# Kernel tuning notes

Hardware: AMD Instinct MI355X
Metric: run time of the kernel (lower is better)

The kernel has to match this reference:

```python
import jax, jax.numpy as jnp
import numpy as np

NUM_PM = 254
NUM_VM = 768
SEQ = NUM_PM + NUM_VM + 2  # 1024
H = 8
D = 256
DH = D // H
FF = 1024
L = 3
B = 8
PM_COV = 16
VM_COV = 16


def _ln(x, g, b, eps=1e-5):
    m = jnp.mean(x, axis=-1, keepdims=True)
    v = jnp.mean((x - m) ** 2, axis=-1, keepdims=True)
    return (x - m) * jax.lax.rsqrt(v + eps) * g + b


def setup_inputs() -> dict:
    key = jax.random.key(0)
    ks = jax.random.split(key, 32)
    n = lambda k, s: (jax.random.normal(k, s, dtype=jnp.float32) * 0.02)
    return {
        "vm_states": jax.random.normal(ks[0], (B, NUM_VM, VM_COV), dtype=jnp.float32),
        "num_step_states": jax.random.uniform(ks[1], (B, 1, 1), dtype=jnp.float32),
        "pm_states": jax.random.normal(ks[2], (B, NUM_PM, PM_COV), dtype=jnp.float32),
        "vm_pm_relation": jax.random.randint(ks[3], (B, SEQ - 2, 1), 0, NUM_PM),
        "num_vms_mask": jnp.zeros((B, NUM_VM), dtype=bool),
        "pm_W": n(ks[4], (PM_COV, D)), "pm_b": jnp.zeros((D,), jnp.float32),
        "vm_W": n(ks[5], (VM_COV, D)), "vm_b": jnp.zeros((D,), jnp.float32),
        "Wqkv": n(ks[6], (L, D, 3 * D)), "bqkv": jnp.zeros((L, 3 * D), jnp.float32),
        "Wo": n(ks[7], (L, D, D)), "bo": jnp.zeros((L, D), jnp.float32),
        "ln1_g": jnp.ones((L, D), jnp.float32), "ln1_b": jnp.zeros((L, D), jnp.float32),
        "ln2_g": jnp.ones((L, D), jnp.float32), "ln2_b": jnp.zeros((L, D), jnp.float32),
        "W1": n(ks[8], (L, D, FF)), "b1": jnp.zeros((L, FF), jnp.float32),
        "W2": n(ks[9], (L, FF, D)), "b2": jnp.zeros((L, D), jnp.float32),
        "out_W": n(ks[10], (D, 1)), "out_b": jnp.zeros((1,), jnp.float32),
        "crit_W": n(ks[11], (D, 1)), "crit_b": jnp.zeros((1,), jnp.float32),
    }


def reference(vm_states, num_step_states, pm_states, vm_pm_relation, num_vms_mask,
              pm_W, pm_b, vm_W, vm_b, Wqkv, bqkv, Wo, bo,
              ln1_g, ln1_b, ln2_g, ln2_b, W1, b1, W2, b2,
              out_W, out_b, crit_W, crit_b):
    b = vm_states.shape[0]
    # --- relation-based sparse mask: True = blocked ---
    r = vm_pm_relation[:, :, 0]                              # [b, SEQ-2]
    inner = r[:, :, None] != r[:, None, :]                   # [b, SEQ-2, SEQ-2]
    local = jnp.ones((b, SEQ, SEQ), dtype=bool)
    local = local.at[:, 0, 0].set(False)
    local = local.at[:, -1, -1].set(False)
    local = local.at[:, 1:-1, 1:-1].set(inner)
    pad = jnp.zeros((b, SEQ), dtype=bool).at[:, 1 + NUM_PM:-1].set(num_vms_mask)
    bias = jnp.where(local | pad[:, None, :], -1e9, 0.0)[:, None]  # [b,1,SEQ,SEQ]
    # --- encode ---
    src = jnp.concatenate([jnp.tile(num_step_states, (1, 1, D)),
                           pm_states @ pm_W + pm_b], axis=1)       # [b, NUM_PM+1, D]
    critic_tok = -jnp.ones((b, 1, D), dtype=vm_states.dtype)
    tgt = jnp.concatenate([vm_states @ vm_W + vm_b, critic_tok], axis=1)  # [b, NUM_VM+1, D]
    x = jnp.concatenate([src, tgt], axis=1)                   # [b, SEQ, D]
    scale = 1.0 / np.sqrt(DH)
    for i in range(L):
        # pre-norm masked self-attention
        h = _ln(x, ln1_g[i], ln1_b[i])
        qkv = h @ Wqkv[i] + bqkv[i]
        q, k, v = [t.reshape(b, SEQ, H, DH) for t in jnp.split(qkv, 3, axis=-1)]
        scores = jnp.einsum('bqhd,bkhd->bhqk', q, k) * scale + bias
        attn = jax.nn.softmax(scores, axis=-1)
        o = jnp.einsum('bhqk,bkhd->bqhd', attn, v).reshape(b, SEQ, D)
        x = x + o @ Wo[i] + bo[i]
        # pre-norm gelu FFN
        h2 = _ln(x, ln2_g[i], ln2_b[i])
        x = x + jax.nn.gelu(h2 @ W1[i] + b1[i]) @ W2[i] + b2[i]
    tgt_out = x[:, NUM_PM + 1:]                               # [b, NUM_VM+1, D]
    score = (tgt_out[:, :-1] @ out_W + out_b)[..., 0]         # [b, NUM_VM]
    critic_score = tgt_out[:, -1] @ crit_W + crit_b           # [b, 1]
    return jnp.concatenate([score, critic_score], axis=1)     # [b, NUM_VM+1]
```

## Files before the change

### kernel.cpp

```cpp
#include <hip/hip_runtime.h>
#include <hip/hip_bf16.h>
#include <math.h>

#define NUM_PM 254
#define NUM_VM 768
#define SEQQ   1024
#define NH     8
#define DD     256
#define DH     32
#define FF     1024
#define NB     8
#define MROWS  (NB*SEQQ)

typedef unsigned short u16;
typedef __attribute__((ext_vector_type(8))) short bf16x8;
typedef __attribute__((ext_vector_type(4))) float f32x4;

__device__ __forceinline__ float bf2f(u16 u){
    union { float f; unsigned int i; } c; c.i = ((unsigned int)u) << 16; return c.f;
}
__device__ __forceinline__ u16 f2bf(float f){
    union { float f; unsigned int u; } c; c.f = f;
    unsigned int r = c.u + 0x7FFFu + ((c.u >> 16) & 1u);
    return (u16)(r >> 16);
}
__device__ __forceinline__ float gelu_tanh(float x){
    float x3 = x*x*x;
    float t = tanhf(0.7978845608028654f*(x + 0.044715f*x3));
    return 0.5f*x*(1.0f+t);
}

#define GLOAD16(gp, lp) __builtin_amdgcn_global_load_lds( \
    (const __attribute__((address_space(1))) void*)(gp), \
    (__attribute__((address_space(3))) void*)(lp), 16, 0, 0)

__global__ void prologue_kernel(const float* __restrict__ Wqkv, const float* __restrict__ Wo,
                                const float* __restrict__ W1,   const float* __restrict__ W2,
                                u16* __restrict__ wq, u16* __restrict__ wo,
                                u16* __restrict__ w1, u16* __restrict__ w2,
                                const int* __restrict__ rel, const unsigned char* __restrict__ mask,
                                int* __restrict__ kcnt, int* __restrict__ koff, int* __restrict__ kmem,
                                int* __restrict__ pcnt, int* __restrict__ poff, int* __restrict__ pmem,
                                const float* __restrict__ vm_states,
                                const float* __restrict__ num_step,
                                const float* __restrict__ pm_states,
                                const float* __restrict__ pm_W, const float* __restrict__ pm_b,
                                const float* __restrict__ vm_W, const float* __restrict__ vm_b,
                                const float* __restrict__ g, const float* __restrict__ beta,
                                float* __restrict__ x, u16* __restrict__ h,
                                float* __restrict__ outz)
{
    __shared__ float t[32][33];
    __shared__ int cntS[256], offS[256], wsum4[4];
    __shared__ int memS[1040];
    int bid = blockIdx.x;
    int tid = threadIdx.x;
    if (bid < 2304){
        int id = bid;
        const float* in; u16* out; int K, N, layer, tile;
        if (id < 576)       { in=Wqkv; out=wq; K=256;  N=768;  layer=id/192; tile=id%192; }
        else if (id < 768)  { id-=576;  in=Wo; out=wo; K=256;  N=256;  layer=id/64;  tile=id%64;  }
        else if (id < 1536) { id-=768;  in=W1; out=w1; K=256;  N=1024; layer=id/256; tile=id%256; }
        else                { id-=1536; in=W2; out=w2; K=1024; N=256;  layer=id/256; tile=id%256; }
        int ntx = N/32;
        int n0 = (tile % ntx)*32, k0 = (tile / ntx)*32;
        size_t lofs = (size_t)layer * K * N;
        int tx = tid & 31, ty = tid >> 5;
        #pragma unroll
        for (int i=0;i<4;i++)
            t[ty + i*8][tx] = in[lofs + (size_t)(k0 + ty + i*8)*N + n0 + tx];
        __syncthreads();
        #pragma unroll
        for (int i=0;i<4;i++)
            out[lofs + (size_t)(n0 + ty + i*8)*K + k0 + tx] = f2bf(t[tx][ty + i*8]);
    } else if (bid < 2312){
        int b = bid - 2304;
        cntS[tid] = 0;
        __syncthreads();
        int myc[4], myp[4];
        bool mykey[4];
        #pragma unroll
        for (int si=0; si<4; si++){
            int s = si*256 + tid;
            bool mid = (s != 0) && (s != SEQQ-1);
            myc[si] = -1; mykey[si] = false;
            if (mid){
                int cc = rel[b*(SEQQ-2) + s-1];
                myc[si] = cc;
                bool masked = (s >= 1+NUM_PM) && mask[b*NUM_VM + (s-1-NUM_PM)];
                if (!masked){ mykey[si] = true; myp[si] = atomicAdd(&cntS[cc], 1); }
            }
        }
        __syncthreads();
        {
            int v = cntS[tid];
            int incl = v;
            #pragma unroll
            for (int d=1; d<64; d<<=1){
                int n = __shfl_up(incl, d);
                if ((tid & 63) >= d) incl += n;
            }
            offS[tid] = incl - v;
            if ((tid & 63) == 63) wsum4[tid>>6] = incl;
        }
        __syncthreads();
        {
            int w = tid >> 6, base = 0;
            #pragma unroll
            for (int i=0;i<4;i++) if (i < w) base += wsum4[i];
            offS[tid] += base;
        }
        __syncthreads();
        #pragma unroll
        for (int si=0; si<4; si++){
            if (mykey[si]){
                int s = si*256 + tid;
                int pos = offS[myc[si]] + myp[si];
                memS[pos] = s;
                kmem[b*SEQQ + pos] = s;
            }
        }
        kcnt[b*256 + tid] = cntS[tid];
        koff[b*256 + tid] = offS[tid];
        __syncthreads();
        #pragma unroll
        for (int si=0; si<4; si++){
            int s = si*256 + tid;
            if (myc[si] >= 0){
                int c = myc[si];
                int cnt = cntS[c], off = offS[c];
                pcnt[b*SEQQ + s] = cnt;
                poff[b*SEQQ + s] = b*SEQQ + off;
                int mrow[16];
                #pragma unroll
                for (int j=0;j<16;j++)
                    mrow[j] = (j < cnt) ? memS[off + j] : s;
                int4* prow = (int4*)&pmem[(size_t)(b*SEQQ + s)*16];
                prow[0] = (int4){mrow[0], mrow[1], mrow[2], mrow[3]};
                prow[1] = (int4){mrow[4], mrow[5], mrow[6], mrow[7]};
                prow[2] = (int4){mrow[8], mrow[9], mrow[10],mrow[11]};
                prow[3] = (int4){mrow[12],mrow[13],mrow[14],mrow[15]};
            }
        }
        #pragma unroll
        for (int si=0; si<4; si++){
            int idx = si*256 + tid;
            if (idx < 769) outz[b*769 + idx] = 0.f;
        }
    } else {
        int row = (bid - 2312)*4 + (tid>>6);
        int lane = tid & 63;
        int b = row >> 10, s = row & 1023;
        int col = lane*4;
        float4 out;
        if (s == 0){
            float v = num_step[b]; out = (float4){v,v,v,v};
        } else if (s == SEQQ-1){
            out = (float4){-1.f,-1.f,-1.f,-1.f};
        } else {
            const float* in; const float* W; const float* bias;
            if (s <= NUM_PM){ in = pm_states + (size_t)(b*NUM_PM + s-1)*16; W = pm_W; bias = pm_b; }
            else            { in = vm_states + (size_t)(b*NUM_VM + (s-1-NUM_PM))*16; W = vm_W; bias = vm_b; }
            float4 i0 = *(const float4*)in,      i1 = *(const float4*)(in+4);
            float4 i2 = *(const float4*)(in+8),  i3 = *(const float4*)(in+12);
            float in16[16] = {i0.x,i0.y,i0.z,i0.w, i1.x,i1.y,i1.z,i1.w,
                              i2.x,i2.y,i2.z,i2.w, i3.x,i3.y,i3.z,i3.w};
            out = *(const float4*)&bias[col];
            #pragma unroll
            for (int k=0;k<16;k++){
                float4 w4 = *(const float4*)&W[k*DD + col];
                out.x = fmaf(in16[k], w4.x, out.x);
                out.y = fmaf(in16[k], w4.y, out.y);
                out.z = fmaf(in16[k], w4.z, out.z);
                out.w = fmaf(in16[k], w4.w, out.w);
            }
        }
        *(float4*)&x[(size_t)row*DD + col] = out;
        float s1 = out.x+out.y+out.z+out.w;
        float s2 = fmaf(out.x,out.x, fmaf(out.y,out.y, fmaf(out.z,out.z, out.w*out.w)));
        #pragma unroll
        for (int off=1; off<64; off<<=1){ s1 += __shfl_xor(s1,off); s2 += __shfl_xor(s2,off); }
        float m    = s1*(1.0f/DD);
        float var  = s2*(1.0f/DD) - m*m;
        float rstd = rsqrtf(var + 1e-5f);
        float4 g4 = *(const float4*)&g[col];
        float4 b4 = *(const float4*)&beta[col];
        short4 o;
        o.x = (short)f2bf((out.x-m)*rstd*g4.x + b4.x);
        o.y = (short)f2bf((out.y-m)*rstd*g4.y + b4.y);
        o.z = (short)f2bf((out.z-m)*rstd*g4.z + b4.z);
        o.w = (short)f2bf((out.w-m)*rstd*g4.w + b4.w);
        *(short4*)&h[(size_t)row*DD + col] = o;
    }
}

__global__ void ln_kernel(const float* __restrict__ x, const float* __restrict__ g,
                          const float* __restrict__ bta, u16* __restrict__ out)
{
    int row = blockIdx.x*4 + (threadIdx.x>>6);
    int lane = threadIdx.x & 63;
    const float4 v = *(const float4*)&x[(size_t)row*DD + lane*4];
    float s1 = v.x+v.y+v.z+v.w;
    float s2 = fmaf(v.x,v.x, fmaf(v.y,v.y, fmaf(v.z,v.z, v.w*v.w)));
    #pragma unroll
    for (int off=1; off<64; off<<=1){ s1 += __shfl_xor(s1,off); s2 += __shfl_xor(s2,off); }
    float m    = s1*(1.0f/DD);
    float var  = s2*(1.0f/DD) - m*m;
    float rstd = rsqrtf(var + 1e-5f);
    float4 g4 = *(const float4*)&g[lane*4];
    float4 b4 = *(const float4*)&bta[lane*4];
    short4 o;
    o.x = (short)f2bf((v.x-m)*rstd*g4.x + b4.x);
    o.y = (short)f2bf((v.y-m)*rstd*g4.y + b4.y);
    o.z = (short)f2bf((v.z-m)*rstd*g4.z + b4.z);
    o.w = (short)f2bf((v.w-m)*rstd*g4.w + b4.w);
    *(short4*)&out[(size_t)row*DD + lane*4] = o;
}

__launch_bounds__(256)
__global__ void qgemm_kernel(const u16* __restrict__ A, const u16* __restrict__ Bt,
                             const float* __restrict__ bias, u16* __restrict__ C,
                             int N, int K)
{
    __shared__ u16 As[2][64][32];
    __shared__ u16 Bs[2][128][32];
    int tid = threadIdx.x;
    int wid = tid >> 6, lane = tid & 63;
    int wr = wid >> 1, wc = wid & 1;
    int row0 = blockIdx.y*64, col0 = blockIdx.x*128;
    int l15 = lane & 15, lh = lane >> 4;

    const u16* Ag = A  + (size_t)(row0 + wid*16 + (lane>>2))*K + (lane&3)*8;
    const u16* Bg = Bt + (size_t)(col0 + wid*32 + (lane>>2))*K + (lane&3)*8;

#define STAGE_Q(buf, k0) do{ \
    GLOAD16(Ag + (k0),          &As[buf][wid*16][0]);    \
    GLOAD16(Bg + (k0),          &Bs[buf][wid*32][0]);    \
    GLOAD16(Bg + (k0) + 16*K,   &Bs[buf][wid*32+16][0]); }while(0)

    f32x4 acc[2][4] = {};
    int nk = K >> 5;
    STAGE_Q(0, 0);
    __syncthreads();
    for (int kt = 0; kt < nk; kt++){
        int cur = kt & 1;
        if (kt+1 < nk) STAGE_Q(cur^1, (kt+1)*32);
        bf16x8 af[2], bfv[4];
        #pragma unroll
        for (int i=0;i<2;i++)
            af[i] = *(const bf16x8*)&As[cur][wr*32 + i*16 + l15][lh*8];
        #pragma unroll
        for (int j=0;j<4;j++)
            bfv[j] = *(const bf16x8*)&Bs[cur][wc*64 + j*16 + l15][lh*8];
        #pragma unroll
        for (int i=0;i<2;i++)
            #pragma unroll
            for (int j=0;j<4;j++)
                acc[i][j] = __builtin_amdgcn_mfma_f32_16x16x32_bf16(af[i], bfv[j], acc[i][j], 0,0,0);
        __syncthreads();
    }
#undef STAGE_Q

    #pragma unroll
    for (int i=0;i<2;i++){
        #pragma unroll
        for (int j=0;j<4;j++){
            int col = col0 + wc*64 + j*16 + l15;
            float bb = bias[col];
            #pragma unroll
            for (int r=0;r<4;r++){
                int row = row0 + wr*32 + i*16 + lh*4 + r;
                C[(size_t)row*N + col] = f2bf(acc[i][j][r] + bb);
            }
        }
    }
}

__launch_bounds__(256)
__global__ void mgemm_kernel(const u16* __restrict__ A, const u16* __restrict__ Bt,
                             const float* __restrict__ bias, u16* __restrict__ C,
                             int N, int K)
{
    __shared__ u16 As[2][128][32];
    __shared__ u16 Bs[2][128][32];
    int tid = threadIdx.x;
    int wid = tid >> 6, lane = tid & 63;
    int wr = wid >> 1, wc = wid & 1;
    int row0 = blockIdx.y*128, col0 = blockIdx.x*128;
    int l15 = lane & 15, lh = lane >> 4;

    const u16* Ag = A  + (size_t)(row0 + wid*32 + (lane>>2))*K + (lane&3)*8;
    const u16* Bg = Bt + (size_t)(col0 + wid*32 + (lane>>2))*K + (lane&3)*8;

#define STAGE_M(buf, k0) do{ \
    GLOAD16(Ag + (k0),          &As[buf][wid*32][0]);    \
    GLOAD16(Ag + (k0) + 16*K,   &As[buf][wid*32+16][0]); \
    GLOAD16(Bg + (k0),          &Bs[buf][wid*32][0]);    \
    GLOAD16(Bg + (k0) + 16*K,   &Bs[buf][wid*32+16][0]); }while(0)

    f32x4 acc[4][4] = {};
    int nk = K >> 5;
    STAGE_M(0, 0);
    __syncthreads();
    for (int kt = 0; kt < nk; kt++){
        int cur = kt & 1;
        if (kt+1 < nk) STAGE_M(cur^1, (kt+1)*32);
        bf16x8 af[4], bfv[4];
        #pragma unroll
        for (int f=0; f<4; f++){
            af[f]  = *(const bf16x8*)&As[cur][wr*64 + f*16 + l15][lh*8];
            bfv[f] = *(const bf16x8*)&Bs[cur][wc*64 + f*16 + l15][lh*8];
        }
        #pragma unroll
        for (int i=0;i<4;i++)
            #pragma unroll
            for (int j=0;j<4;j++)
                acc[i][j] = __builtin_amdgcn_mfma_f32_16x16x32_bf16(af[i], bfv[j], acc[i][j], 0,0,0);
        __syncthreads();
    }
#undef STAGE_M

    #pragma unroll
    for (int i=0;i<4;i++){
        #pragma unroll
        for (int j=0;j<4;j++){
            int col = col0 + wc*64 + j*16 + l15;
            float bb = bias[col];
            #pragma unroll
            for (int r=0;r<4;r++){
                int row = row0 + wr*64 + i*16 + lh*4 + r;
                C[(size_t)row*N + col] = f2bf(gelu_tanh(acc[i][j][r] + bb));
            }
        }
    }
}

template<int HEAD>
__launch_bounds__(256)
__global__ void mgemm64_kernel(const u16* __restrict__ A, const u16* __restrict__ Bt,
                               const float* __restrict__ bias, float* __restrict__ x,
                               const float* __restrict__ out_W, const float* __restrict__ out_b,
                               const float* __restrict__ crit_W, const float* __restrict__ crit_b,
                               float* __restrict__ out, int K)
{
    __shared__ u16 As[2][64][32];
    __shared__ u16 Bs[2][64][32];
    int tid = threadIdx.x;
    int wid = tid >> 6, lane = tid & 63;
    int wr = wid >> 1, wc = wid & 1;
    int row0 = blockIdx.y*64, col0 = blockIdx.x*64;
    int l15 = lane & 15, lh = lane >> 4;

    const u16* Ag = A  + (size_t)(row0 + wid*16 + (lane>>2))*K + (lane&3)*8;
    const u16* Bg = Bt + (size_t)(col0 + wid*16 + (lane>>2))*K + (lane&3)*8;

#define STAGE_S(buf, k0) do{ \
    GLOAD16(Ag + (k0), &As[buf][wid*16][0]); \
    GLOAD16(Bg + (k0), &Bs[buf][wid*16][0]); }while(0)

    f32x4 acc[2][2] = {};
    int nk = K >> 5;
    STAGE_S(0, 0);
    __syncthreads();
    for (int kt = 0; kt < nk; kt++){
        int cur = kt & 1;
        if (kt+1 < nk) STAGE_S(cur^1, (kt+1)*32);
        bf16x8 af[2], bfv[2];
        #pragma unroll
        for (int i=0;i<2;i++)
            af[i] = *(const bf16x8*)&As[cur][wr*32 + i*16 + l15][lh*8];
        #pragma unroll
        for (int j=0;j<2;j++)
            bfv[j] = *(const bf16x8*)&Bs[cur][wc*32 + j*16 + l15][lh*8];
        #pragma unroll
        for (int i=0;i<2;i++)
            #pragma unroll
            for (int j=0;j<2;j++)
                acc[i][j] = __builtin_amdgcn_mfma_f32_16x16x32_bf16(af[i], bfv[j], acc[i][j], 0,0,0);
        __syncthreads();
    }
#undef STAGE_S

    #pragma unroll
    for (int i=0;i<2;i++){
        #pragma unroll
        for (int r=0;r<4;r++){
            int row = row0 + wr*32 + i*16 + lh*4 + r;
            float hp = 0.f;
            int s = row & 1023;
            #pragma unroll
            for (int j=0;j<2;j++){
                int col = col0 + wc*32 + j*16 + l15;
                size_t idx = (size_t)row*DD + col;
                float v = acc[i][j][r] + bias[col] + x[idx];
                x[idx] = v;
                if (HEAD){
                    float w = (s == 1023) ? crit_W[col] : out_W[col];
                    hp = fmaf(v, w, hp);
                }
            }
            if (HEAD && s >= 1 + NUM_PM){
                hp += __shfl_xor(hp, 1);
                hp += __shfl_xor(hp, 2);
                hp += __shfl_xor(hp, 4);
                hp += __shfl_xor(hp, 8);
                if (l15 == 0){
                    int b = row >> 10;
                    int jj = (s == 1023) ? 768 : (s - (1 + NUM_PM));
                    float add = hp;
                    if (blockIdx.x == 0 && wc == 0)
                        add += (s == 1023) ? crit_b[0] : out_b[0];
                    atomicAdd(&out[b*769 + jj], add);
                }
            }
        }
    }
}

__launch_bounds__(256)
__global__ void attn_kernel(const u16* __restrict__ qkv,
                            const int* __restrict__ pcnt, const int* __restrict__ pmem,
                            const int* __restrict__ poff, const int* __restrict__ kmem,
                            u16* __restrict__ o)
{
    int gq = blockIdx.x*4 + (threadIdx.x >> 6);
    int lane = threadIdx.x & 63;
    int b = gq >> 10, s = gq & 1023;
    const float scale = 0.17677669529663687f;

    if (s == 0 || s == SEQQ-1){
        const u16* vrow = qkv + (size_t)gq*768 + 512 + lane*4;
        *(short4*)(o + (size_t)gq*DD + lane*4) = *(const short4*)vrow;
        return;
    }

    const u16* qb = qkv + (size_t)gq*768 + lane*4;
    short4 q4i = *(const short4*)qb;
    float qx = bf2f((u16)q4i.x)*scale, qy = bf2f((u16)q4i.y)*scale,
          qz = bf2f((u16)q4i.z)*scale, qw = bf2f((u16)q4i.w)*scale;

    int cnt = pcnt[gq];
    const int4* prow = (const int4*)&pmem[(size_t)gq*16];
    int4 m0 = prow[0], m1 = prow[1], m2 = prow[2], m3 = prow[3];

    float m_run = -1e30f, l_run = 0.f;
    float ax=0.f, ay=0.f, az=0.f, aw=0.f;

#define ACHUNK(BASE, MV) do{                                              \
    if ((BASE) < cnt){                                                    \
        short4 k4[4], v4[4];                                              \
        const int mi0=(MV).x, mi1=(MV).y, mi2=(MV).z, mi3=(MV).w;         \
        const u16* kb0 = qkv + (size_t)(b*SEQQ + mi0)*768 + 256 + lane*4; \
        const u16* kb1 = qkv + (size_t)(b*SEQQ + mi1)*768 + 256 + lane*4; \
        const u16* kb2 = qkv + (size_t)(b*SEQQ + mi2)*768 + 256 + lane*4; \
        const u16* kb3 = qkv + (size_t)(b*SEQQ + mi3)*768 + 256 + lane*4; \
        k4[0]=*(const short4*)kb0; v4[0]=*(const short4*)(kb0+256);       \
        k4[1]=*(const short4*)kb1; v4[1]=*(const short4*)(kb1+256);       \
        k4[2]=*(const short4*)kb2; v4[2]=*(const short4*)(kb2+256);       \
        k4[3]=*(const short4*)kb3; v4[3]=*(const short4*)(kb3+256);       \
        _Pragma("unroll")                                                 \
        for (int k=0;k<4;k++){                                            \
            if ((BASE) + k < cnt){                                        \
                float sc = qx*bf2f((u16)k4[k].x) + qy*bf2f((u16)k4[k].y)  \
                         + qz*bf2f((u16)k4[k].z) + qw*bf2f((u16)k4[k].w); \
                sc += __shfl_xor(sc, 1);                                  \
                sc += __shfl_xor(sc, 2);                                  \
                sc += __shfl_xor(sc, 4);                                  \
                float mn = fmaxf(m_run, sc);                              \
                float corr = __expf(m_run - mn);                          \
                float p = __expf(sc - mn);                                \
                l_run = l_run*corr + p;                                   \
                ax = ax*corr + p*bf2f((u16)v4[k].x);                      \
                ay = ay*corr + p*bf2f((u16)v4[k].y);                      \
                az = az*corr + p*bf2f((u16)v4[k].z);                      \
                aw = aw*corr + p*bf2f((u16)v4[k].w);                      \
                m_run = mn;                                               \
            }                                                             \
        }                                                                 \
    } }while(0)

    if (cnt <= 16){
        ACHUNK(0,  m0);
        ACHUNK(4,  m1);
        ACHUNK(8,  m2);
        ACHUNK(12, m3);
    } else {
        const int* klist = kmem + poff[gq];
        for (int j0 = 0; j0 < cnt; j0 += 4){
            short4 k4[4], v4[4];
            #pragma unroll
            for (int k=0;k<4;k++){
                int jj = j0 + k; jj = (jj < cnt) ? jj : (cnt-1);
                int mi = klist[jj];
                const u16* kb = qkv + (size_t)(b*SEQQ + mi)*768 + 256 + lane*4;
                k4[k] = *(const short4*)kb;
                v4[k] = *(const short4*)(kb + 256);
            }
            #pragma unroll
            for (int k=0;k<4;k++){
                if (j0 + k < cnt){
                    float sc = qx*bf2f((u16)k4[k].x) + qy*bf2f((u16)k4[k].y)
                             + qz*bf2f((u16)k4[k].z) + qw*bf2f((u16)k4[k].w);
                    sc += __shfl_xor(sc, 1);
                    sc += __shfl_xor(sc, 2);
                    sc += __shfl_xor(sc, 4);
                    float mn = fmaxf(m_run, sc);
                    float corr = __expf(m_run - mn);
                    float p = __expf(sc - mn);
                    l_run = l_run*corr + p;
                    ax = ax*corr + p*bf2f((u16)v4[k].x);
                    ay = ay*corr + p*bf2f((u16)v4[k].y);
                    az = az*corr + p*bf2f((u16)v4[k].z);
                    aw = aw*corr + p*bf2f((u16)v4[k].w);
                    m_run = mn;
                }
            }
        }
    }
#undef ACHUNK

    float inv = (l_run > 0.f) ? 1.0f/l_run : 0.f;
    u16* orow = o + (size_t)gq*DD + lane*4;
    short4 outv;
    outv.x = (short)f2bf(ax*inv); outv.y = (short)f2bf(ay*inv);
    outv.z = (short)f2bf(az*inv); outv.w = (short)f2bf(aw*inv);
    *(short4*)orow = outv;
}

extern "C" void kernel_launch(void* const* d_in, const int* in_sizes, int n_in,
                              void* d_out, int out_size, void* d_ws, size_t ws_size,
                              hipStream_t stream)
{
    const float* vm_states = (const float*)d_in[0];
    const float* num_step  = (const float*)d_in[1];
    const float* pm_states = (const float*)d_in[2];
    const int*   rel       = (const int*)d_in[3];
    const unsigned char* mask = (const unsigned char*)d_in[4];
    const float* pm_W = (const float*)d_in[5];
    const float* pm_b = (const float*)d_in[6];
    const float* vm_W = (const float*)d_in[7];
    const float* vm_b = (const float*)d_in[8];
    const float* Wqkv = (const float*)d_in[9];
    const float* bqkv = (const float*)d_in[10];
    const float* Wo   = (const float*)d_in[11];
    const float* bo   = (const float*)d_in[12];
    const float* ln1g = (const float*)d_in[13];
    const float* ln1b = (const float*)d_in[14];
    const float* ln2g = (const float*)d_in[15];
    const float* ln2b = (const float*)d_in[16];
    const float* W1   = (const float*)d_in[17];
    const float* b1   = (const float*)d_in[18];
    const float* W2   = (const float*)d_in[19];
    const float* b2   = (const float*)d_in[20];
    const float* out_W = (const float*)d_in[21];
    const float* out_b = (const float*)d_in[22];
    const float* crit_W = (const float*)d_in[23];
    const float* crit_b = (const float*)d_in[24];

    char* ws = (char*)d_ws;
    const size_t MB = 1024*1024;
    float* x    = (float*)(ws);
    u16*   hbuf = (u16*)(ws + 8*MB);
    u16*   aout = (u16*)(ws + 12*MB);
    u16*   qkv  = (u16*)(ws + 16*MB);
    u16*   ff1  = (u16*)(ws + 28*MB);
    u16*   wq   = (u16*)(ws + 44*MB);
    u16*   wo   = wq + (size_t)3*768*256;
    u16*   w1   = wo + (size_t)3*256*256;
    u16*   w2   = w1 + (size_t)3*1024*256;
    int*   kcnt = (int*)(ws + 50*MB);
    int*   koff = kcnt + NB*256;
    int*   kmem = koff + NB*256;
    int*   pcnt = kmem + NB*SEQQ;
    int*   poff = pcnt + MROWS;
    int*   pmem = poff + MROWS;

    prologue_kernel<<<4360, 256, 0, stream>>>(Wqkv, Wo, W1, W2, wq, wo, w1, w2,
                                              rel, mask, kcnt, koff, kmem, pcnt, poff, pmem,
                                              vm_states, num_step, pm_states,
                                              pm_W, pm_b, vm_W, vm_b,
                                              ln1g, ln1b, x, hbuf, (float*)d_out);
    for (int i=0;i<3;i++){
        qgemm_kernel<<<dim3(768/128, MROWS/64),256,0,stream>>>(
            hbuf, wq + (size_t)i*768*256, bqkv + i*768, qkv, 768, 256);
        attn_kernel<<<MROWS/4, 256, 0, stream>>>(qkv, pcnt, pmem, poff, kmem, aout);
        mgemm64_kernel<0><<<dim3(256/64, MROWS/64),256,0,stream>>>(
            aout, wo + (size_t)i*256*256, bo + i*DD, x,
            nullptr, nullptr, nullptr, nullptr, nullptr, 256);
        ln_kernel<<<MROWS/4,256,0,stream>>>(x, ln2g + i*DD, ln2b + i*DD, hbuf);
        mgemm_kernel<<<dim3(1024/128, MROWS/128),256,0,stream>>>(
            hbuf, w1 + (size_t)i*1024*256, b1 + i*FF, ff1, 1024, 256);
        if (i < 2){
            mgemm64_kernel<0><<<dim3(256/64, MROWS/64),256,0,stream>>>(
                ff1, w2 + (size_t)i*256*1024, b2 + i*DD, x,
                nullptr, nullptr, nullptr, nullptr, nullptr, 1024);
            ln_kernel<<<MROWS/4,256,0,stream>>>(x, ln1g + (i+1)*DD, ln1b + (i+1)*DD, hbuf);
        } else {
            mgemm64_kernel<1><<<dim3(256/64, MROWS/64),256,0,stream>>>(
                ff1, w2 + (size_t)i*256*1024, b2 + i*DD, x,
                out_W, out_b, crit_W, crit_b, (float*)d_out, 1024);
        }
    }
}
```

Before: 332.4 us.

## Triple-buffer GEMM shared-memory staging with vmcnt waits and single barrier

```diff
diff --git a/kernel.cpp b/kernel.cpp
--- a/kernel.cpp
+++ b/kernel.cpp
@@ -217,13 +217,15 @@
     *(short4*)&out[(size_t)row*DD + lane*4] = o;
 }
 
+#define VMWAIT(N) asm volatile("s_waitcnt vmcnt(" #N ")" ::: "memory")
+
 __launch_bounds__(256)
 __global__ void qgemm_kernel(const u16* __restrict__ A, const u16* __restrict__ Bt,
                              const float* __restrict__ bias, u16* __restrict__ C,
                              int N, int K)
 {
-    __shared__ u16 As[2][64][32];
-    __shared__ u16 Bs[2][128][32];
+    __shared__ u16 As[3][64][32];
+    __shared__ u16 Bs[3][128][32];
     int tid = threadIdx.x;
     int wid = tid >> 6, lane = tid & 63;
     int wr = wid >> 1, wc = wid & 1;
@@ -241,10 +243,12 @@
     f32x4 acc[2][4] = {};
     int nk = K >> 5;
     STAGE_Q(0, 0);
-    __syncthreads();
+    STAGE_Q(1, 32);
     for (int kt = 0; kt < nk; kt++){
-        int cur = kt & 1;
-        if (kt+1 < nk) STAGE_Q(cur^1, (kt+1)*32);
+        int cur = kt % 3;
+        if (kt+1 < nk) VMWAIT(3);
+        else           VMWAIT(0);
+        __builtin_amdgcn_s_barrier();
         bf16x8 af[2], bfv[4];
         #pragma unroll
         for (int i=0;i<2;i++)
@@ -252,12 +256,12 @@
         #pragma unroll
         for (int j=0;j<4;j++)
             bfv[j] = *(const bf16x8*)&Bs[cur][wc*64 + j*16 + l15][lh*8];
+        if (kt+2 < nk) STAGE_Q((kt+2)%3, (kt+2)*32);
         #pragma unroll
         for (int i=0;i<2;i++)
             #pragma unroll
             for (int j=0;j<4;j++)
                 acc[i][j] = __builtin_amdgcn_mfma_f32_16x16x32_bf16(af[i], bfv[j], acc[i][j], 0,0,0);
-        __syncthreads();
     }
 #undef STAGE_Q
 
@@ -281,8 +285,8 @@
                              const float* __restrict__ bias, u16* __restrict__ C,
                              int N, int K)
 {
-    __shared__ u16 As[2][128][32];
-    __shared__ u16 Bs[2][128][32];
+    __shared__ u16 As[3][128][32];
+    __shared__ u16 Bs[3][128][32];
     int tid = threadIdx.x;
     int wid = tid >> 6, lane = tid & 63;
     int wr = wid >> 1, wc = wid & 1;
@@ -301,22 +305,24 @@
     f32x4 acc[4][4] = {};
     int nk = K >> 5;
     STAGE_M(0, 0);
-    __syncthreads();
+    STAGE_M(1, 32);
     for (int kt = 0; kt < nk; kt++){
-        int cur = kt & 1;
-        if (kt+1 < nk) STAGE_M(cur^1, (kt+1)*32);
+        int cur = kt % 3;
+        if (kt+1 < nk) VMWAIT(4);
+        else           VMWAIT(0);
+        __builtin_amdgcn_s_barrier();
         bf16x8 af[4], bfv[4];
         #pragma unroll
         for (int f=0; f<4; f++){
             af[f]  = *(const bf16x8*)&As[cur][wr*64 + f*16 + l15][lh*8];
             bfv[f] = *(const bf16x8*)&Bs[cur][wc*64 + f*16 + l15][lh*8];
         }
+        if (kt+2 < nk) STAGE_M((kt+2)%3, (kt+2)*32);
         #pragma unroll
         for (int i=0;i<4;i++)
             #pragma unroll
             for (int j=0;j<4;j++)
                 acc[i][j] = __builtin_amdgcn_mfma_f32_16x16x32_bf16(af[i], bfv[j], acc[i][j], 0,0,0);
-        __syncthreads();
     }
 #undef STAGE_M
 
@@ -343,8 +349,8 @@
                                const float* __restrict__ crit_W, const float* __restrict__ crit_b,
                                float* __restrict__ out, int K)
 {
-    __shared__ u16 As[2][64][32];
-    __shared__ u16 Bs[2][64][32];
+    __shared__ u16 As[3][64][32];
+    __shared__ u16 Bs[3][64][32];
     int tid = threadIdx.x;
     int wid = tid >> 6, lane = tid & 63;
     int wr = wid >> 1, wc = wid & 1;
@@ -361,10 +367,12 @@
     f32x4 acc[2][2] = {};
     int nk = K >> 5;
     STAGE_S(0, 0);
-    __syncthreads();
+    STAGE_S(1, 32);
     for (int kt = 0; kt < nk; kt++){
-        int cur = kt & 1;
-        if (kt+1 < nk) STAGE_S(cur^1, (kt+1)*32);
+        int cur = kt % 3;
+        if (kt+1 < nk) VMWAIT(2);
+        else           VMWAIT(0);
+        __builtin_amdgcn_s_barrier();
         bf16x8 af[2], bfv[2];
         #pragma unroll
         for (int i=0;i<2;i++)
@@ -372,12 +380,12 @@
         #pragma unroll
         for (int j=0;j<2;j++)
             bfv[j] = *(const bf16x8*)&Bs[cur][wc*32 + j*16 + l15][lh*8];
+        if (kt+2 < nk) STAGE_S((kt+2)%3, (kt+2)*32);
         #pragma unroll
         for (int i=0;i<2;i++)
             #pragma unroll
             for (int j=0;j<2;j++)
                 acc[i][j] = __builtin_amdgcn_mfma_f32_16x16x32_bf16(af[i], bfv[j], acc[i][j], 0,0,0);
-        __syncthreads();
     }
 #undef STAGE_S
 
```

Result: faster. 324.9 us (-2.2%).
